# Performance work log

Hardware: AMD Instinct MI355X
Metric: run time of the kernel (lower is better)

The kernel has to match this reference:

```python
import jax, jax.numpy as jnp
import numpy as np
from jax import lax

NSAMPLE = 16
NEG_SLOPE = 0.1


def leaky(x):
    return jnp.where(x >= 0, x, NEG_SLOPE * x)


def setup_inputs() -> dict:
    key = jax.random.key(0)
    ks = jax.random.split(key, 8)
    B, N1, N2, D = 4, 4096, 4096, 64
    C_in, C_mid, C_out = D + D + 3, 128, 128  # 131 -> 128 -> 128
    xyz1 = jax.random.normal(ks[0], (B, 3, N1), jnp.float32)
    xyz2 = jax.random.normal(ks[1], (B, 3, N2), jnp.float32)
    points1 = jax.random.normal(ks[2], (B, D, N1), jnp.float32)
    points2 = jax.random.normal(ks[3], (B, D, N2), jnp.float32)
    W1 = jax.random.normal(ks[4], (C_mid, C_in), jnp.float32) * 0.05
    b1 = jnp.zeros((C_mid,), jnp.float32)
    W2 = jax.random.normal(ks[5], (C_out, C_mid), jnp.float32) * 0.05
    b2 = jnp.zeros((C_out,), jnp.float32)
    return {"xyz1": xyz1, "xyz2": xyz2, "points1": points1, "points2": points2,
            "W1": W1, "b1": b1, "W2": W2, "b2": b2}


def reference(xyz1, xyz2, points1, points2, W1, b1, W2, b2):
    B, _, N1 = xyz1.shape
    x1 = jnp.transpose(xyz1, (0, 2, 1))      # [B,N1,3]
    x2 = jnp.transpose(xyz2, (0, 2, 1))      # [B,N2,3]
    p1 = jnp.transpose(points1, (0, 2, 1))   # [B,N1,D1]
    p2 = jnp.transpose(points2, (0, 2, 1))   # [B,N2,D2]

    # knn_point: k smallest squared distances from each x1 point into x2
    d2 = (jnp.sum(x1 * x1, -1)[:, :, None]
          + jnp.sum(x2 * x2, -1)[:, None, :]
          - 2.0 * jnp.einsum('bnc,bmc->bnm', x1, x2))  # [B,N1,N2]
    _, knn_idx = lax.top_k(-d2, NSAMPLE)     # [B,N1,K]

    bidx = jnp.arange(B)[:, None, None]
    neighbor_xyz = x2[bidx, knn_idx]         # [B,N1,K,3]
    direction_xyz = neighbor_xyz - x1[:, :, None, :]
    gp2 = p2[bidx, knn_idx]                  # [B,N1,K,D2]
    gp1 = jnp.broadcast_to(p1[:, :, None, :], (B, N1, NSAMPLE, p1.shape[-1]))
    feat = jnp.concatenate([gp1, gp2, direction_xyz], axis=-1)  # [B,N1,K,131]

    h = leaky(jnp.einsum('oc,bnkc->bnko', W1, feat) + b1)
    h = leaky(jnp.einsum('oc,bnkc->bnko', W2, h) + b2)           # [B,N1,K,C_out]

    dist = jnp.maximum(jnp.linalg.norm(direction_xyz, axis=3), 1e-10)  # [B,N1,K]
    inv = 1.0 / dist
    weights = inv / jnp.sum(inv, axis=2, keepdims=True)          # [B,N1,K]

    cost = jnp.einsum('bnk,bnko->bon', weights, h)               # [B,C_out,N1]
    return cost
```

## Files before the change

### kernel.cpp

```cpp
#include <hip/hip_runtime.h>

typedef unsigned short u16;
typedef unsigned int u32;
typedef unsigned long long u64;
typedef __bf16 bf16x8 __attribute__((ext_vector_type(8)));
typedef float f32x4 __attribute__((ext_vector_type(4)));

#define MFMA16(a, b, c) __builtin_amdgcn_mfma_f32_16x16x32_bf16(a, b, c, 0, 0, 0)

static __device__ __forceinline__ u16 f2bf(float f) {
  union { float f; u32 u; } v; v.f = f;
  u32 u = v.u;
  u32 r = (u + 0x7FFFu + ((u >> 16) & 1u)) >> 16;
  return (u16)r;
}

static __device__ __forceinline__ bf16x8 ld16(const u16* p) {
  return __builtin_bit_cast(bf16x8, *(const uint4*)p);
}

static __device__ __forceinline__ u64 u64min(u64 a, u64 b) { return a < b ? a : b; }

static __device__ __forceinline__ u64 bitonic64(u64 v, int lane) {
#pragma unroll
  for (int k = 2; k <= 64; k <<= 1) {
#pragma unroll
    for (int j = k >> 1; j > 0; j >>= 1) {
      u64 o = __shfl_xor(v, j, 64);
      bool up = ((lane & k) == 0);
      bool lower = ((lane & j) == 0);
      u64 mn = v < o ? v : o;
      u64 mx = v < o ? o : v;
      v = (lower == up) ? mn : mx;
    }
  }
  return v;
}

static __device__ __forceinline__ void bitonic64_2(u64& a, u64& b, int lane) {
#pragma unroll
  for (int k = 2; k <= 64; k <<= 1) {
#pragma unroll
    for (int j = k >> 1; j > 0; j >>= 1) {
      u64 oa = __shfl_xor(a, j, 64);
      u64 ob = __shfl_xor(b, j, 64);
      bool up = ((lane & k) == 0);
      bool lower = ((lane & j) == 0);
      bool sel = (lower == up);
      u64 mna = a < oa ? a : oa;
      u64 mxa = a < oa ? oa : a;
      u64 mnb = b < ob ? b : ob;
      u64 mxb = b < ob ? ob : b;
      a = sel ? mna : mxa;
      b = sel ? mnb : mxb;
    }
  }
}

static __device__ __forceinline__ void bitonic64f_2(float& a, float& b, int lane) {
#pragma unroll
  for (int k = 2; k <= 64; k <<= 1) {
#pragma unroll
    for (int j = k >> 1; j > 0; j >>= 1) {
      float oa = __shfl_xor(a, j, 64);
      float ob = __shfl_xor(b, j, 64);
      bool up = ((lane & k) == 0);
      bool lower = ((lane & j) == 0);
      bool sel = (lower == up);
      float mna = fminf(a, oa), mxa = fmaxf(a, oa);
      float mnb = fminf(b, ob), mxb = fmaxf(b, ob);
      a = sel ? mna : mxa;
      b = sel ? mnb : mxb;
    }
  }
}

static __device__ __forceinline__ u32 fkey(float f) {
  u32 bb = __float_as_uint(f);
  u32 sgn = (u32)((int)bb >> 31);
  return bb ^ (sgn | 0x80000000u);
}

static __device__ __forceinline__ float d2of(float x, float y, float z, float s1,
                                             f32x4 c) {
  float dt = __builtin_fmaf(z, c[2], __builtin_fmaf(y, c[1], __fmul_rn(x, c[0])));
  return __fsub_rn(__fadd_rn(s1, c[3]), __fmul_rn(2.0f, dt));
}

__global__ __launch_bounds__(512, 2) void knn_prep(
    const float* __restrict__ xyz1, const float* __restrict__ xyz2,
    const float* __restrict__ points1, const float* __restrict__ points2,
    const float* __restrict__ W1, const float* __restrict__ W2,
    u16* __restrict__ p1t, u16* __restrict__ p2t,
    u16* __restrict__ W1b, u16* __restrict__ W2b,
    int* __restrict__ knn) {
  __shared__ __align__(16) char LB[65536];
  f32x4* candL = (f32x4*)LB;
  u16* tile = (u16*)LB;
  __shared__ u64 surv[8][2][64];
  const int t = threadIdx.x;
  const int lane = t & 63;
  const int w = t >> 6;
  const int g = blockIdx.x;

  if (g < 72) {
    int i = g * 512 + t;
    if (i < 128 * 160) {
      int r = i / 160, c = i - r * 160;
      W1b[i] = (c < 131) ? f2bf(W1[r * 131 + c]) : (u16)0;
    } else {
      int u = i - 128 * 160;
      W2b[u] = f2bf(W2[u]);
    }
  }

  {
    const float* src = (g < 256) ? points1 : points2;
    u16* dst = (g < 256) ? p1t : p2t;
    const int gb = g & 255;
    const int tb = gb >> 6;
    const int n0 = (gb & 63) << 6;
    const float* sp = src + ((size_t)tb << 18);
#pragma unroll
    for (int i = 0; i < 8; i++) {
      int d = (i << 3) + (t >> 6);
      int n = t & 63;
      tile[n * 66 + d] = f2bf(sp[((size_t)d << 12) + n0 + n]);
    }
    __syncthreads();
    u16* dp = dst + ((size_t)(tb * 4096 + n0) << 6);
#pragma unroll
    for (int i = 0; i < 4; i++) {
      int n = (i << 4) + (t >> 5);
      int dp2 = t & 31;
      *(u32*)(dp + n * 64 + (dp2 << 1)) = *(const u32*)(tile + n * 66 + (dp2 << 1));
    }
  }
  __syncthreads();

  const int b = g >> 7;
  const int rbase = (g & 127) << 5;
  const float* X1 = xyz1 + b * 12288;
  const float* X2 = xyz2 + b * 12288;
#pragma unroll
  for (int i = 0; i < 8; i++) {
    int m = i * 512 + t;
    float x = X2[m], y = X2[4096 + m], z = X2[8192 + m];
    float s2 = __fadd_rn(__fadd_rn(__fmul_rn(x, x), __fmul_rn(y, y)),
                         __fmul_rn(z, z));
    f32x4 pk = {x, y, z, s2};
    candL[m] = pk;
  }
  __syncthreads();

#pragma unroll 1
  for (int pr = 0; pr < 2; pr++) {
    const int n0 = rbase + (w << 2) + (pr << 1);
    const int n1 = n0 + 1;
    const int row0 = b * 4096 + n0;
    const int row1 = row0 + 1;
    const float x0 = X1[n0], y0 = X1[4096 + n0], z0 = X1[8192 + n0];
    const float x1 = X1[n1], y1 = X1[4096 + n1], z1 = X1[8192 + n1];
    const float s10 = __fadd_rn(__fadd_rn(__fmul_rn(x0, x0), __fmul_rn(y0, y0)),
                                __fmul_rn(z0, z0));
    const float s11 = __fadd_rn(__fadd_rn(__fmul_rn(x1, x1), __fmul_rn(y1, y1)),
                                __fmul_rn(z1, z1));

    float fm0 = 3e38f, fm1 = 3e38f;
#pragma unroll 8
    for (int j = 0; j < 64; j++) {
      f32x4 c = candL[(j << 6) + lane];
      fm0 = fminf(fm0, d2of(x0, y0, z0, s10, c));
      fm1 = fminf(fm1, d2of(x1, y1, z1, s11, c));
    }

    bitonic64f_2(fm0, fm1, lane);
    float tau0 = __shfl(fm0, 15, 64);
    float tau1 = __shfl(fm1, 15, 64);

    u32 base0 = 0, base1 = 0;
#pragma unroll 8
    for (int j = 0; j < 64; j++) {
      const int m = (j << 6) + lane;
      f32x4 c = candL[m];
      float d0 = d2of(x0, y0, z0, s10, c);
      float d1 = d2of(x1, y1, z1, s11, c);
      bool p0 = d0 <= tau0;
      bool p1 = d1 <= tau1;
      u64 mk0 = __ballot(p0);
      u64 mk1 = __ballot(p1);
      if (mk0) {
        if (p0) {
          u32 pre = __builtin_amdgcn_mbcnt_lo((u32)mk0, 0u);
          pre = __builtin_amdgcn_mbcnt_hi((u32)(mk0 >> 32), pre);
          u32 slot = base0 + pre;
          if (slot < 64u) surv[w][0][slot] = ((u64)fkey(d0) << 32) | (u32)m;
        }
        base0 += (u32)__popcll(mk0);
      }
      if (mk1) {
        if (p1) {
          u32 pre = __builtin_amdgcn_mbcnt_lo((u32)mk1, 0u);
          pre = __builtin_amdgcn_mbcnt_hi((u32)(mk1 >> 32), pre);
          u32 slot = base1 + pre;
          if (slot < 64u) surv[w][1][slot] = ((u64)fkey(d1) << 32) | (u32)m;
        }
        base1 += (u32)__popcll(mk1);
      }
    }
    const u32 S0 = base0, S1 = base1;

    if (S0 <= 64 && S1 <= 64) {
      u64 v0 = (lane < (int)S0) ? surv[w][0][lane] : ~0ull;
      u64 v1 = (lane < (int)S1) ? surv[w][1][lane] : ~0ull;
      bitonic64_2(v0, v1, lane);
      if (lane < 16) {
        knn[row0 * 16 + lane] = (int)(v0 & 0xFFFFFFFFull);
        knn[row1 * 16 + lane] = (int)(v1 & 0xFFFFFFFFull);
      }
    } else {
#pragma unroll 1
      for (int p = 0; p < 2; p++) {
        const u32 S = p ? S1 : S0;
        const int row = p ? row1 : row0;
        const float xx = p ? x1 : x0, yy = p ? y1 : y0, zz = p ? z1 : z0;
        const float ss = p ? s11 : s10;
        if (S <= 64) {
          u64 v = (lane < (int)S) ? surv[w][p][lane] : ~0ull;
          v = bitonic64(v, lane);
          if (lane < 16) knn[row * 16 + lane] = (int)(v & 0xFFFFFFFFull);
        } else {
          u64 prev = 0;
          for (int rr = 0; rr < 16; rr++) {
            u64 lm = ~0ull;
#pragma unroll 8
            for (int j = 0; j < 64; j++) {
              const int m = (j << 6) + lane;
              f32x4 c = candL[m];
              float d = d2of(xx, yy, zz, ss, c);
              u64 k64 = ((u64)fkey(d) << 32) | (u32)m;
              if (k64 > prev && k64 < lm) lm = k64;
            }
            u64 gm = lm;
#pragma unroll
            for (int off = 32; off; off >>= 1)
              gm = u64min(gm, __shfl_xor(gm, off, 64));
            if (lane == 0) knn[row * 16 + rr] = (int)(gm & 0xFFFFFFFFull);
            prev = gm;
          }
        }
      }
    }
  }
}

__global__ __launch_bounds__(256, 3) void mlp_kernel(
    const float* __restrict__ xyz1, const float* __restrict__ xyz2,
    const u16* __restrict__ p1t, const u16* __restrict__ p2t,
    const int* __restrict__ knn,
    const u16* __restrict__ W1b, const float* __restrict__ b1,
    const u16* __restrict__ W2b, const float* __restrict__ b2,
    float* __restrict__ out) {
  __shared__ __align__(16) u16 F[128 * 168];
  __shared__ __align__(16) float winv[128];
  __shared__ __align__(16) float wnorm[128];
  __shared__ __align__(16) float outbuf[128 * 12];
  const int t = threadIdx.x;
  const int g = blockIdx.x;
  const int b = g >> 9;
  const int rbase = (g & 511) << 3;

  {
    const int m = t >> 1, half = t & 1;
    const int n1 = rbase + (m >> 4);
    const uint4* s1p = (const uint4*)(p1t + ((size_t)(b * 4096 + n1) << 6)) + half * 4;
    uint4* d1p = (uint4*)(F + m * 168) + half * 4;
    d1p[0] = s1p[0]; d1p[1] = s1p[1]; d1p[2] = s1p[2]; d1p[3] = s1p[3];
    const int idx = knn[(((size_t)(b * 4096 + n1)) << 4) + (m & 15)];
    const uint4* s2p = (const uint4*)(p2t + ((size_t)(b * 4096 + idx) << 6)) + half * 4;
    uint4* d2p = (uint4*)(F + m * 168 + 64) + half * 4;
    d2p[0] = s2p[0]; d2p[1] = s2p[1]; d2p[2] = s2p[2]; d2p[3] = s2p[3];
  }
  if (t < 128) {
    const int m = t;
    const int n1 = rbase + (m >> 4);
    const int idx = knn[(((size_t)(b * 4096 + n1)) << 4) + (m & 15)];
    const float* X1 = xyz1 + b * 12288;
    const float* X2 = xyz2 + b * 12288;
    float dx = X2[idx] - X1[n1];
    float dy = X2[4096 + idx] - X1[4096 + n1];
    float dz = X2[8192 + idx] - X1[8192 + n1];
    u32 u0 = (u32)f2bf(dx) | ((u32)f2bf(dy) << 16);
    u32 u1 = (u32)f2bf(dz);
    uint4 pk = make_uint4(u0, u1, 0u, 0u);
    *(uint4*)(F + m * 168 + 128) = pk;
    float d = sqrtf(dx * dx + dy * dy + dz * dz);
    winv[m] = 1.0f / fmaxf(d, 1e-10f);
  } else {
    const int m = t - 128;
    uint4 zz = make_uint4(0u, 0u, 0u, 0u);
    uint4* zp = (uint4*)(F + m * 168 + 136);
    zp[0] = zz; zp[1] = zz; zp[2] = zz; zp[3] = zz;
  }
  __syncthreads();

  if (t < 128) {
    const int r = t >> 4;
    float s = 0.f;
#pragma unroll
    for (int k = 0; k < 16; k++) s += winv[(r << 4) + k];
    wnorm[t] = winv[t] / s;
  }

  const int lane = t & 63;
  const int wid = t >> 6;
  const int l15 = lane & 15;
  const int quad = lane >> 4;
  const int koff = quad << 3;
  const int nbase = wid << 5;

  f32x4 acc[8][2];
  const f32x4 z4 = {0.f, 0.f, 0.f, 0.f};
#pragma unroll
  for (int i = 0; i < 8; i++)
#pragma unroll
    for (int j = 0; j < 2; j++) acc[i][j] = z4;

#pragma unroll
  for (int s = 0; s < 5; s++) {
    bf16x8 bf0 = ld16(W1b + (nbase + l15) * 160 + s * 32 + koff);
    bf16x8 bf1 = ld16(W1b + (nbase + 16 + l15) * 160 + s * 32 + koff);
#pragma unroll
    for (int mt = 0; mt < 8; mt++) {
      bf16x8 a = ld16(F + (mt * 16 + l15) * 168 + s * 32 + koff);
      acc[mt][0] = MFMA16(a, bf0, acc[mt][0]);
      acc[mt][1] = MFMA16(a, bf1, acc[mt][1]);
    }
  }
  __syncthreads();

  {
    const float bv0 = b1[nbase + l15];
    const float bv1 = b1[nbase + 16 + l15];
#pragma unroll
    for (int mt = 0; mt < 8; mt++) {
      u16* hrow = F + (mt * 16 + quad * 4) * 168;
#pragma unroll
      for (int r = 0; r < 4; r++) {
        float zv0 = acc[mt][0][r] + bv0;
        zv0 = (zv0 >= 0.f) ? zv0 : 0.1f * zv0;
        hrow[r * 168 + nbase + l15] = f2bf(zv0);
        float zv1 = acc[mt][1][r] + bv1;
        zv1 = (zv1 >= 0.f) ? zv1 : 0.1f * zv1;
        hrow[r * 168 + nbase + 16 + l15] = f2bf(zv1);
      }
    }
  }
  __syncthreads();

  f32x4 acc2[8][2];
#pragma unroll
  for (int i = 0; i < 8; i++)
#pragma unroll
    for (int j = 0; j < 2; j++) acc2[i][j] = z4;

#pragma unroll
  for (int s = 0; s < 4; s++) {
    bf16x8 bf0 = ld16(W2b + (nbase + l15) * 128 + s * 32 + koff);
    bf16x8 bf1 = ld16(W2b + (nbase + 16 + l15) * 128 + s * 32 + koff);
#pragma unroll
    for (int mt = 0; mt < 8; mt++) {
      bf16x8 a = ld16(F + (mt * 16 + l15) * 168 + s * 32 + koff);
      acc2[mt][0] = MFMA16(a, bf0, acc2[mt][0]);
      acc2[mt][1] = MFMA16(a, bf1, acc2[mt][1]);
    }
  }

  {
    const float bv0 = b2[nbase + l15];
    const float bv1 = b2[nbase + 16 + l15];
#pragma unroll
    for (int mt = 0; mt < 8; mt++) {
      const f32x4 w4 = *(const f32x4*)&wnorm[(mt << 4) + (quad << 2)];
      float p0 = 0.f, p1 = 0.f;
#pragma unroll
      for (int r = 0; r < 4; r++) {
        float zv0 = acc2[mt][0][r] + bv0;
        zv0 = (zv0 >= 0.f) ? zv0 : 0.1f * zv0;
        p0 += zv0 * w4[r];
        float zv1 = acc2[mt][1][r] + bv1;
        zv1 = (zv1 >= 0.f) ? zv1 : 0.1f * zv1;
        p1 += zv1 * w4[r];
      }
      p0 += __shfl_xor(p0, 16); p0 += __shfl_xor(p0, 32);
      p1 += __shfl_xor(p1, 16); p1 += __shfl_xor(p1, 32);
      if (quad == 0) {
        outbuf[(nbase + l15) * 12 + mt] = p0;
        outbuf[(nbase + 16 + l15) * 12 + mt] = p1;
      }
    }
  }
  __syncthreads();
  {
    const int ch = t >> 1, half = t & 1;
    f32x4 v = *(const f32x4*)&outbuf[ch * 12 + (half << 2)];
    float* op = out + (((size_t)(b * 128 + ch)) << 12) + rbase + (half << 2);
    *(f32x4*)op = v;
  }
}

extern "C" void kernel_launch(void* const* d_in, const int* in_sizes, int n_in,
                              void* d_out, int out_size, void* d_ws, size_t ws_size,
                              hipStream_t stream) {
  const float* xyz1 = (const float*)d_in[0];
  const float* xyz2 = (const float*)d_in[1];
  const float* points1 = (const float*)d_in[2];
  const float* points2 = (const float*)d_in[3];
  const float* W1 = (const float*)d_in[4];
  const float* b1 = (const float*)d_in[5];
  const float* W2 = (const float*)d_in[6];
  const float* b2 = (const float*)d_in[7];
  float* out = (float*)d_out;

  char* ws = (char*)d_ws;
  int* knn = (int*)ws;
  u16* p1t = (u16*)(ws + 1048576);
  u16* p2t = (u16*)(ws + 3145728);
  u16* W1b = (u16*)(ws + 5242880);
  u16* W2b = (u16*)(ws + 5283840);

  hipLaunchKernelGGL(knn_prep, dim3(512), dim3(512), 0, stream,
                     xyz1, xyz2, points1, points2, W1, W2, p1t, p2t, W1b, W2b, knn);
  hipLaunchKernelGGL(mlp_kernel, dim3(2048), dim3(256), 0, stream,
                     xyz1, xyz2, p1t, p2t, knn, W1b, b1, W2b, b2, out);
}
```

Before: 143.2 us.

## Double knn block size, radix-select threshold, add 32-wide survivor sort

```diff
diff --git a/kernel.cpp b/kernel.cpp
--- a/kernel.cpp
+++ b/kernel.cpp
@@ -47,28 +47,26 @@
       bool up = ((lane & k) == 0);
       bool lower = ((lane & j) == 0);
       bool sel = (lower == up);
-      u64 mna = a < oa ? a : oa;
-      u64 mxa = a < oa ? oa : a;
-      u64 mnb = b < ob ? b : ob;
-      u64 mxb = b < ob ? ob : b;
+      u64 mna = a < oa ? a : oa, mxa = a < oa ? oa : a;
+      u64 mnb = b < ob ? b : ob, mxb = b < ob ? ob : b;
       a = sel ? mna : mxa;
       b = sel ? mnb : mxb;
     }
   }
 }
 
-static __device__ __forceinline__ void bitonic64f_2(float& a, float& b, int lane) {
-#pragma unroll
-  for (int k = 2; k <= 64; k <<= 1) {
+static __device__ __forceinline__ void bitonic32_2(u64& a, u64& b, int lane) {
+#pragma unroll
+  for (int k = 2; k <= 32; k <<= 1) {
 #pragma unroll
     for (int j = k >> 1; j > 0; j >>= 1) {
-      float oa = __shfl_xor(a, j, 64);
-      float ob = __shfl_xor(b, j, 64);
+      u64 oa = __shfl_xor(a, j, 64);
+      u64 ob = __shfl_xor(b, j, 64);
       bool up = ((lane & k) == 0);
       bool lower = ((lane & j) == 0);
       bool sel = (lower == up);
-      float mna = fminf(a, oa), mxa = fmaxf(a, oa);
-      float mnb = fminf(b, ob), mxb = fmaxf(b, ob);
+      u64 mna = a < oa ? a : oa, mxa = a < oa ? oa : a;
+      u64 mnb = b < ob ? b : ob, mxb = b < ob ? ob : b;
       a = sel ? mna : mxa;
       b = sel ? mnb : mxb;
     }
@@ -81,13 +79,18 @@
   return bb ^ (sgn | 0x80000000u);
 }
 
+static __device__ __forceinline__ float ikey(u32 k) {
+  u32 bb = (k & 0x80000000u) ? (k ^ 0x80000000u) : ~k;
+  return __uint_as_float(bb);
+}
+
 static __device__ __forceinline__ float d2of(float x, float y, float z, float s1,
                                              f32x4 c) {
   float dt = __builtin_fmaf(z, c[2], __builtin_fmaf(y, c[1], __fmul_rn(x, c[0])));
   return __fsub_rn(__fadd_rn(s1, c[3]), __fmul_rn(2.0f, dt));
 }
 
-__global__ __launch_bounds__(512, 2) void knn_prep(
+__global__ __launch_bounds__(1024, 2) void knn_prep(
     const float* __restrict__ xyz1, const float* __restrict__ xyz2,
     const float* __restrict__ points1, const float* __restrict__ points2,
     const float* __restrict__ W1, const float* __restrict__ W2,
@@ -97,14 +100,14 @@
   __shared__ __align__(16) char LB[65536];
   f32x4* candL = (f32x4*)LB;
   u16* tile = (u16*)LB;
-  __shared__ u64 surv[8][2][64];
+  __shared__ u64 surv[16][2][64];
   const int t = threadIdx.x;
   const int lane = t & 63;
   const int w = t >> 6;
   const int g = blockIdx.x;
 
-  if (g < 72) {
-    int i = g * 512 + t;
+  if (g < 36) {
+    int i = g * 1024 + t;
     if (i < 128 * 160) {
       int r = i / 160, c = i - r * 160;
       W1b[i] = (c < 131) ? f2bf(W1[r * 131 + c]) : (u16)0;
@@ -122,16 +125,16 @@
     const int n0 = (gb & 63) << 6;
     const float* sp = src + ((size_t)tb << 18);
 #pragma unroll
-    for (int i = 0; i < 8; i++) {
-      int d = (i << 3) + (t >> 6);
+    for (int i = 0; i < 4; i++) {
+      int d = (i << 4) + (t >> 6);
       int n = t & 63;
       tile[n * 66 + d] = f2bf(sp[((size_t)d << 12) + n0 + n]);
     }
     __syncthreads();
     u16* dp = dst + ((size_t)(tb * 4096 + n0) << 6);
 #pragma unroll
-    for (int i = 0; i < 4; i++) {
-      int n = (i << 4) + (t >> 5);
+    for (int i = 0; i < 2; i++) {
+      int n = (i << 5) + (t >> 5);
       int dp2 = t & 31;
       *(u32*)(dp + n * 64 + (dp2 << 1)) = *(const u32*)(tile + n * 66 + (dp2 << 1));
     }
@@ -143,8 +146,8 @@
   const float* X1 = xyz1 + b * 12288;
   const float* X2 = xyz2 + b * 12288;
 #pragma unroll
-  for (int i = 0; i < 8; i++) {
-    int m = i * 512 + t;
+  for (int i = 0; i < 4; i++) {
+    int m = i * 1024 + t;
     float x = X2[m], y = X2[4096 + m], z = X2[8192 + m];
     float s2 = __fadd_rn(__fadd_rn(__fmul_rn(x, x), __fmul_rn(y, y)),
                          __fmul_rn(z, z));
@@ -153,9 +156,8 @@
   }
   __syncthreads();
 
-#pragma unroll 1
-  for (int pr = 0; pr < 2; pr++) {
-    const int n0 = rbase + (w << 2) + (pr << 1);
+  {
+    const int n0 = rbase + (w << 1);
     const int n1 = n0 + 1;
     const int row0 = b * 4096 + n0;
     const int row1 = row0 + 1;
@@ -174,9 +176,19 @@
       fm1 = fminf(fm1, d2of(x1, y1, z1, s11, c));
     }
 
-    bitonic64f_2(fm0, fm1, lane);
-    float tau0 = __shfl(fm0, 15, 64);
-    float tau1 = __shfl(fm1, 15, 64);
+    const u32 k0 = fkey(fm0), k1 = fkey(fm1);
+    u32 lo0 = 0u, hi0 = 0xFFFFFFFFu, lo1 = 0u, hi1 = 0xFFFFFFFFu;
+#pragma unroll
+    for (int it = 0; it < 32; it++) {
+      u32 md0 = lo0 + ((hi0 - lo0) >> 1);
+      u32 md1 = lo1 + ((hi1 - lo1) >> 1);
+      bool ge0 = __popcll(__ballot(k0 <= md0)) >= 16;
+      bool ge1 = __popcll(__ballot(k1 <= md1)) >= 16;
+      hi0 = ge0 ? md0 : hi0;  lo0 = ge0 ? lo0 : md0 + 1;
+      hi1 = ge1 ? md1 : hi1;  lo1 = ge1 ? lo1 : md1 + 1;
+    }
+    const float tau0 = ikey(hi0);
+    const float tau1 = ikey(hi1);
 
     u32 base0 = 0, base1 = 0;
 #pragma unroll 8
@@ -210,7 +222,16 @@
     }
     const u32 S0 = base0, S1 = base1;
 
-    if (S0 <= 64 && S1 <= 64) {
+    const u32 Smax = max(S0, S1);
+    if (Smax <= 32) {
+      u64 v0 = (lane < (int)S0) ? surv[w][0][lane] : ~0ull;
+      u64 v1 = (lane < (int)S1) ? surv[w][1][lane] : ~0ull;
+      bitonic32_2(v0, v1, lane);
+      if (lane < 16) {
+        knn[row0 * 16 + lane] = (int)(v0 & 0xFFFFFFFFull);
+        knn[row1 * 16 + lane] = (int)(v1 & 0xFFFFFFFFull);
+      }
+    } else if (Smax <= 64) {
       u64 v0 = (lane < (int)S0) ? surv[w][0][lane] : ~0ull;
       u64 v1 = (lane < (int)S1) ? surv[w][1][lane] : ~0ull;
       bitonic64_2(v0, v1, lane);
@@ -429,7 +450,7 @@
   u16* W1b = (u16*)(ws + 5242880);
   u16* W2b = (u16*)(ws + 5283840);
 
-  hipLaunchKernelGGL(knn_prep, dim3(512), dim3(512), 0, stream,
+  hipLaunchKernelGGL(knn_prep, dim3(512), dim3(1024), 0, stream,
                      xyz1, xyz2, points1, points2, W1, W2, p1t, p2t, W1b, W2b, knn);
   hipLaunchKernelGGL(mlp_kernel, dim3(2048), dim3(256), 0, stream,
                      xyz1, xyz2, p1t, p2t, knn, W1b, b1, W2b, b2, out);
```

Result: no change. 143.6 us (+0.3%).
